# Optimization experiments

Measured on AMD Instinct MI355X. Metric: run time of the kernel, lower is better.

Reference implementation:

```python
import jax, jax.numpy as jnp
import numpy as np

EMB = 1024
NH = 16
DH = EMB // NH
SCALE = np.sqrt(EMB).astype(np.float32)  # module scales by sqrt(emb_dim), not sqrt(d_head)


def setup_inputs() -> dict:
    key = jax.random.key(0)
    ks = jax.random.split(key, 9)
    s = 1.0 / np.sqrt(EMB)
    return {
        "a": jax.random.normal(ks[0], (4, 2048, EMB), jnp.float32),
        "Wq": jax.random.normal(ks[1], (EMB, EMB), jnp.float32) * s,
        "bq": jnp.zeros((EMB,), jnp.float32),
        "Wk": jax.random.normal(ks[2], (EMB, EMB), jnp.float32) * s,
        "bk": jnp.zeros((EMB,), jnp.float32),
        "Wv": jax.random.normal(ks[3], (EMB, EMB), jnp.float32) * s,
        "bv": jnp.zeros((EMB,), jnp.float32),
        "Wo": jax.random.normal(ks[4], (EMB, EMB), jnp.float32) * s,
        "bo": jnp.zeros((EMB,), jnp.float32),
    }


def reference(a, Wq, bq, Wk, bk, Wv, bv, Wo, bo):
    N, S, _ = a.shape
    # Q/K/V projections (self-attention: b is None -> b = a)
    Q = (a @ Wq + bq).reshape(N, S, NH, DH).transpose(0, 2, 1, 3)  # [N,H,A,D]
    K = (a @ Wk + bk).reshape(N, S, NH, DH).transpose(0, 2, 1, 3)  # [N,H,B,D]
    V = (a @ Wv + bv).reshape(N, S, NH, DH).transpose(0, 2, 1, 3)  # [N,H,B,D]
    score = jnp.einsum('nhad,nhbd->nhab', Q, K) / SCALE
    score = jax.nn.softmax(score, axis=-1)
    out = jnp.einsum('nhab,nhbd->nhad', score, V)                  # [N,H,A,D]
    out = out.transpose(0, 2, 1, 3).reshape(N, S, EMB)
    return out @ Wo + bo
```

## Files before the change

kernel.cpp:

```cpp
#include <hip/hip_runtime.h>
#include <hip/hip_bf16.h>
#include <stdint.h>

typedef __attribute__((ext_vector_type(8))) short short8v;
typedef __attribute__((ext_vector_type(4))) float float4v;

#define GLDS16(gp, lp) __builtin_amdgcn_global_load_lds( \
    (const __attribute__((address_space(1))) void*)(gp),  \
    (__attribute__((address_space(3))) void*)(lp), 16, 0, 0)

#if __has_builtin(__builtin_amdgcn_exp2f)
#define EXP2(x) __builtin_amdgcn_exp2f(x)
#else
#define EXP2(x) exp2f(x)
#endif

#define LOG2E 1.4426950408889634f

__global__ __launch_bounds__(256) void cast_a_kernel(
    const float* __restrict__ src, __hip_bfloat16* __restrict__ dst, int n4) {
  int i = blockIdx.x * blockDim.x + threadIdx.x;
  if (i < n4) {
    float4 v = ((const float4*)src)[i];
    union { __hip_bfloat16 h[4]; ushort4 u; } p;
    p.h[0] = __float2bfloat16(v.x);
    p.h[1] = __float2bfloat16(v.y);
    p.h[2] = __float2bfloat16(v.z);
    p.h[3] = __float2bfloat16(v.w);
    ((ushort4*)dst)[i] = p.u;
  }
}

__global__ __launch_bounds__(256) void transpose_cast_kernel(
    const float* __restrict__ W, __hip_bfloat16* __restrict__ WT) {
  __shared__ float t[32][33];
  int tx = threadIdx.x & 31, ty = threadIdx.x >> 5;
  int r0 = blockIdx.y * 32, c0 = blockIdx.x * 32;
#pragma unroll
  for (int i = 0; i < 4; ++i) {
    int r = ty + i * 8;
    t[r][tx] = W[(size_t)(r0 + r) * 1024 + c0 + tx];
  }
  __syncthreads();
#pragma unroll
  for (int i = 0; i < 4; ++i) {
    int r = ty + i * 8;
    WT[(size_t)(c0 + r) * 1024 + r0 + tx] = __float2bfloat16(t[tx][r]);
  }
}

template <int MODE>
__global__ __launch_bounds__(256, 2) void gemm_kernel(
    const __hip_bfloat16* __restrict__ A, const __hip_bfloat16* __restrict__ BT,
    const float* __restrict__ bias, void* __restrict__ C, float scale) {
  __shared__ char lds[16384];
  const int tid = threadIdx.x;
  const int l = tid & 63, w = tid >> 6;
  const int g = l >> 4, cc = l & 15;
  const int m0 = blockIdx.x * 128, n0 = blockIdx.y * 128;
  const int wm = w >> 1, wn = w & 1;

  float4v acc[4][4];
#pragma unroll
  for (int m = 0; m < 4; ++m)
#pragma unroll
    for (int n = 0; n < 4; ++n) acc[m][n] = (float4v){0.f, 0.f, 0.f, 0.f};

  for (int kt = 0; kt < 32; ++kt) {
#pragma unroll
    for (int j = 0; j < 2; ++j) {
      int ci = (w * 2 + j) * 64 + l;
      int row = ci >> 2, ko = (ci & 3) * 16;
      GLDS16((const char*)A + (size_t)(m0 + row) * 2048 + kt * 64 + ko,
             lds + ci * 16);
      GLDS16((const char*)BT + (size_t)(n0 + row) * 2048 + kt * 64 + ko,
             lds + 8192 + ci * 16);
    }
    __syncthreads();
    short8v af[4], bf[4];
#pragma unroll
    for (int m = 0; m < 4; ++m)
      af[m] = *(const short8v*)(lds + ((wm * 64 + m * 16 + cc) * 32 + g * 8) * 2);
#pragma unroll
    for (int n = 0; n < 4; ++n)
      bf[n] = *(const short8v*)(lds + 8192 + ((wn * 64 + n * 16 + cc) * 32 + g * 8) * 2);
#pragma unroll
    for (int m = 0; m < 4; ++m)
#pragma unroll
      for (int n = 0; n < 4; ++n)
        acc[m][n] = __builtin_amdgcn_mfma_f32_16x16x32_bf16(af[m], bf[n], acc[m][n], 0, 0, 0);
    __syncthreads();
  }

  if (MODE == 0) {
    float* out = (float*)C;
#pragma unroll
    for (int m = 0; m < 4; ++m) {
      int row = m0 + wm * 64 + m * 16 + g * 4;
#pragma unroll
      for (int n = 0; n < 4; ++n) {
        int col = n0 + wn * 64 + n * 16 + cc;
        float b = bias[col];
#pragma unroll
        for (int r = 0; r < 4; ++r)
          out[(size_t)(row + r) * 1024 + col] = acc[m][n][r] + b;
      }
    }
  } else if (MODE == 1) {
    __hip_bfloat16* out = (__hip_bfloat16*)C;
#pragma unroll
    for (int m = 0; m < 4; ++m) {
#pragma unroll
      for (int n = 0; n < 4; ++n) {
        int col = n0 + wn * 64 + n * 16 + cc;
        float b = bias[col];
        int h = col >> 6, d = col & 63;
#pragma unroll
        for (int r = 0; r < 4; ++r) {
          int grow = m0 + wm * 64 + m * 16 + g * 4 + r;
          int nb = grow >> 11, s = grow & 2047;
          out[((size_t)(nb * 16 + h) * 2048 + s) * 64 + d] =
              __float2bfloat16((acc[m][n][r] + b) * scale);
        }
      }
    }
  } else {
    __hip_bfloat16* out = (__hip_bfloat16*)C;
#pragma unroll
    for (int m = 0; m < 4; ++m) {
#pragma unroll
      for (int n = 0; n < 4; ++n) {
        int col = n0 + wn * 64 + n * 16 + cc;
        int nb = col >> 11, key = col & 2047;
        int kp = (key & ~31) | ((key & 12) << 1) | (((key >> 4) & 1) << 2) | (key & 3);
#pragma unroll
        for (int r = 0; r < 4; ++r) {
          int row = m0 + wm * 64 + m * 16 + g * 4 + r;
          int h = row >> 6, d = row & 63;
          out[((size_t)((nb * 16 + h) * 64 + d)) * 2048 + kp] =
              __float2bfloat16(acc[m][n][r] + bias[row]);
        }
      }
    }
  }
}

__global__ __launch_bounds__(256, 4) void attn_kernel(
    const __hip_bfloat16* __restrict__ Q,
    const __hip_bfloat16* __restrict__ K,
    const __hip_bfloat16* __restrict__ VT,
    __hip_bfloat16* __restrict__ AO) {
  __shared__ char sK[2][8192];
  __shared__ char sV[2][8192];
  const int tid = threadIdx.x;
  const int l = tid & 63, w = tid >> 6;
  const int g = l >> 4, cc = l & 15;
  const int bid = blockIdx.x;
  const int nbid = (bid & 7) * 128 + (bid >> 3);
  const int bx = nbid & 15, nh = nbid >> 4;
  const int q0 = bx * 128 + w * 32;
  const char* Kb = (const char*)(K + (size_t)nh * 131072);
  const char* Vb = (const char*)(VT + (size_t)nh * 131072);
  const __hip_bfloat16* Qb = Q + (size_t)nh * 131072;

  short8v qf[2][2];
#pragma unroll
  for (int qg = 0; qg < 2; ++qg)
#pragma unroll
    for (int dh = 0; dh < 2; ++dh)
      qf[qg][dh] = *(const short8v*)(Qb + (size_t)(q0 + qg * 16 + cc) * 64 + dh * 32 + g * 8);

  int koff[4][2], voff[4][2];
#pragma unroll
  for (int kg = 0; kg < 4; ++kg)
#pragma unroll
    for (int dh = 0; dh < 2; ++dh) {
      int row = kg * 16 + cc;
      koff[kg][dh] = (row * 128 + dh * 64 + g * 16) ^ ((row & 7) << 4);
    }
#pragma unroll
  for (int f = 0; f < 4; ++f)
#pragma unroll
    for (int hh = 0; hh < 2; ++hh) {
      int d = f * 16 + cc;
      voff[f][hh] = (d * 128 + hh * 64 + g * 16) ^ ((d & 7) << 4);
    }
  int stK[2], stV[2], stD[2];
#pragma unroll
  for (int ii = 0; ii < 2; ++ii) {
    int i = w + ii * 4;
    int s = i * 1024 + l * 16;
    int r = s >> 7;
    int off = (s & 127) ^ ((r & 7) << 4);
    stK[ii] = r * 128 + off;
    stV[ii] = r * 4096 + off;
    stD[ii] = i * 1024;
  }

  const short8v fone = {16256, 16256, 16256, 16256, 16256, 16256, 16256, 16256};

  float mr[2] = {0.f, 0.f}, lr[2] = {0.f, 0.f};
  float4v oacc[2][4];
#pragma unroll
  for (int qg = 0; qg < 2; ++qg)
#pragma unroll
    for (int f = 0; f < 4; ++f) oacc[qg][f] = (float4v){0.f, 0.f, 0.f, 0.f};

#define STAGE(b, ktv)                                                         \
  {                                                                           \
    _Pragma("unroll")                                                         \
    for (int ii = 0; ii < 2; ++ii) {                                          \
      GLDS16(Kb + (size_t)(ktv) * 8192 + stK[ii], sK[b] + stD[ii]);           \
      GLDS16(Vb + (size_t)(ktv) * 128 + stV[ii], sV[b] + stD[ii]);            \
    }                                                                         \
  }

  STAGE(0, 0);
  asm volatile("s_waitcnt vmcnt(0)" ::: "memory");
  __builtin_amdgcn_s_barrier();

#pragma unroll 2
  for (int kt = 0; kt < 32; ++kt) {
    const int cur = kt & 1;
    if (kt < 31) STAGE(cur ^ 1, kt + 1);
    const char* sKc = sK[cur];
    const char* sVc = sV[cur];

    short8v kf[4][2];
#pragma unroll
    for (int kg = 0; kg < 4; ++kg)
#pragma unroll
      for (int dh = 0; dh < 2; ++dh)
        kf[kg][dh] = *(const short8v*)(sKc + koff[kg][dh]);

    float4v sv[2][4];
    __builtin_amdgcn_s_setprio(1);
#pragma unroll
    for (int qg = 0; qg < 2; ++qg) {
      float nm = -mr[qg];
#pragma unroll
      for (int kg = 0; kg < 4; ++kg) {
        float4v z = (float4v){nm, nm, nm, nm};
        z = __builtin_amdgcn_mfma_f32_16x16x32_bf16(kf[kg][0], qf[qg][0], z, 0, 0, 0);
        sv[qg][kg] = __builtin_amdgcn_mfma_f32_16x16x32_bf16(kf[kg][1], qf[qg][1], z, 0, 0, 0);
      }
    }
    __builtin_amdgcn_s_setprio(0);

    short8v pf[2][2];
#pragma unroll
    for (int qg = 0; qg < 2; ++qg) {
      float t0 = fmaxf(fmaxf(sv[qg][0][0], sv[qg][0][1]), sv[qg][0][2]);
      float t1 = fmaxf(fmaxf(sv[qg][0][3], sv[qg][1][0]), sv[qg][1][1]);
      float t2 = fmaxf(fmaxf(sv[qg][1][2], sv[qg][1][3]), sv[qg][2][0]);
      float t3 = fmaxf(fmaxf(sv[qg][2][1], sv[qg][2][2]), sv[qg][2][3]);
      float t4 = fmaxf(fmaxf(sv[qg][3][0], sv[qg][3][1]), sv[qg][3][2]);
      float t5 = fmaxf(sv[qg][3][3], fmaxf(t0, t1));
      float vm = fmaxf(fmaxf(t2, t3), fmaxf(t4, t5));
      vm = fmaxf(vm, __shfl_xor(vm, 16));
      vm = fmaxf(vm, __shfl_xor(vm, 32));
      if (__any(vm > 11.54f)) {
        float rsc = EXP2(-vm);
        mr[qg] += vm;
        lr[qg] *= rsc;
#pragma unroll
        for (int f = 0; f < 4; ++f)
#pragma unroll
          for (int r = 0; r < 4; ++r) oacc[qg][f][r] *= rsc;
#pragma unroll
        for (int kg = 0; kg < 4; ++kg)
#pragma unroll
          for (int r = 0; r < 4; ++r) sv[qg][kg][r] -= vm;
      }
#pragma unroll
      for (int kg = 0; kg < 4; ++kg)
#pragma unroll
        for (int r = 0; r < 4; ++r) sv[qg][kg][r] = EXP2(sv[qg][kg][r]);
#pragma unroll
      for (int hh = 0; hh < 2; ++hh) {
        union { __hip_bfloat16 h[8]; short8v v8; } pk;
#pragma unroll
        for (int j = 0; j < 4; ++j) {
          pk.h[j]     = __float2bfloat16(sv[qg][2 * hh][j]);
          pk.h[4 + j] = __float2bfloat16(sv[qg][2 * hh + 1][j]);
        }
        pf[qg][hh] = pk.v8;
      }
      float4v t = (float4v){0.f, 0.f, 0.f, 0.f};
      t = __builtin_amdgcn_mfma_f32_16x16x32_bf16(fone, pf[qg][0], t, 0, 0, 0);
      t = __builtin_amdgcn_mfma_f32_16x16x32_bf16(fone, pf[qg][1], t, 0, 0, 0);
      lr[qg] += t[0];
    }

    __builtin_amdgcn_s_setprio(1);
#pragma unroll
    for (int f = 0; f < 4; ++f)
#pragma unroll
      for (int hh = 0; hh < 2; ++hh) {
        short8v vk = *(const short8v*)(sVc + voff[f][hh]);
#pragma unroll
        for (int qg = 0; qg < 2; ++qg)
          oacc[qg][f] = __builtin_amdgcn_mfma_f32_16x16x32_bf16(vk, pf[qg][hh], oacc[qg][f], 0, 0, 0);
      }
    __builtin_amdgcn_s_setprio(0);

    asm volatile("s_waitcnt vmcnt(0)" ::: "memory");
    __builtin_amdgcn_s_barrier();
  }
#undef STAGE

  int nb = nh >> 4, h = nh & 15;
#pragma unroll
  for (int qg = 0; qg < 2; ++qg) {
    float inv = 1.f / lr[qg];
    int qrow = q0 + qg * 16 + cc;
#pragma unroll
    for (int f = 0; f < 4; ++f)
#pragma unroll
      for (int r = 0; r < 4; ++r) {
        int d = f * 16 + g * 4 + r;
        AO[(size_t)(nb * 2048 + qrow) * 1024 + h * 64 + d] =
            __float2bfloat16(oacc[qg][f][r] * inv);
      }
  }
}

extern "C" void kernel_launch(void* const* d_in, const int* in_sizes, int n_in,
                              void* d_out, int out_size, void* d_ws, size_t ws_size,
                              hipStream_t stream) {
  const float* a  = (const float*)d_in[0];
  const float* Wq = (const float*)d_in[1];
  const float* bq = (const float*)d_in[2];
  const float* Wk = (const float*)d_in[3];
  const float* bk = (const float*)d_in[4];
  const float* Wv = (const float*)d_in[5];
  const float* bv = (const float*)d_in[6];
  const float* Wo = (const float*)d_in[7];
  const float* bo = (const float*)d_in[8];

  char* ws = (char*)d_ws;
  __hip_bfloat16* aB  = (__hip_bfloat16*)(ws);
  __hip_bfloat16* WqT = (__hip_bfloat16*)(ws + (16ull << 20));
  __hip_bfloat16* WkT = (__hip_bfloat16*)(ws + (18ull << 20));
  __hip_bfloat16* WvT = (__hip_bfloat16*)(ws + (20ull << 20));
  __hip_bfloat16* WoT = (__hip_bfloat16*)(ws + (22ull << 20));
  __hip_bfloat16* Qh  = (__hip_bfloat16*)(ws + (24ull << 20));
  __hip_bfloat16* Kh  = (__hip_bfloat16*)(ws + (40ull << 20));
  __hip_bfloat16* Vt  = (__hip_bfloat16*)(ws + (56ull << 20));
  __hip_bfloat16* AOb = (__hip_bfloat16*)(ws + (72ull << 20));

  cast_a_kernel<<<8192, 256, 0, stream>>>(a, aB, 8192 * 1024 / 4);
  dim3 tg(32, 32);
  transpose_cast_kernel<<<tg, 256, 0, stream>>>(Wq, WqT);
  transpose_cast_kernel<<<tg, 256, 0, stream>>>(Wk, WkT);
  transpose_cast_kernel<<<tg, 256, 0, stream>>>(Wv, WvT);
  transpose_cast_kernel<<<tg, 256, 0, stream>>>(Wo, WoT);

  dim3 gg(64, 8);
  gemm_kernel<1><<<gg, 256, 0, stream>>>(aB, WqT, bq, (void*)Qh, LOG2E / 32.f);
  gemm_kernel<1><<<gg, 256, 0, stream>>>(aB, WkT, bk, (void*)Kh, 1.f);
  dim3 gv(8, 64);
  gemm_kernel<2><<<gv, 256, 0, stream>>>(WvT, aB, bv, (void*)Vt, 1.f);

  attn_kernel<<<1024, 256, 0, stream>>>(Qh, Kh, Vt, AOb);

  gemm_kernel<0><<<gg, 256, 0, stream>>>(AOb, WoT, bo, d_out, 1.f);
}
```

Before: 215.9 us.

## Fuse QKV projections into one GEMM, batch weight transposes, triple-buffer attention

The four weight transpose launches become one launch with a z dimension, and the three Q/K/V projection GEMMs become a single launch over a concatenated weight. The V output is now computed as aB·Wv with packed 4-element bf16 stores into the permuted transposed layout. Both GEMMs get a swizzled block order for better L2 locality. The attention kernel moves from double to triple buffering with a partial vmcnt wait and one barrier per iteration, at the cost of more LDS and occupancy lowered from 4 to 3 blocks.

```diff
diff --git a/kernel.cpp b/kernel.cpp
--- a/kernel.cpp
+++ b/kernel.cpp
@@ -31,9 +31,14 @@
   }
 }
 
-__global__ __launch_bounds__(256) void transpose_cast_kernel(
-    const float* __restrict__ W, __hip_bfloat16* __restrict__ WT) {
+__global__ __launch_bounds__(256) void transpose4_kernel(
+    const float* __restrict__ Wq, const float* __restrict__ Wk,
+    const float* __restrict__ Wv, const float* __restrict__ Wo,
+    __hip_bfloat16* __restrict__ Wcat, __hip_bfloat16* __restrict__ WoT) {
   __shared__ float t[32][33];
+  const int z = blockIdx.z;
+  const float* W = (z == 0) ? Wq : (z == 1) ? Wk : (z == 2) ? Wv : Wo;
+  __hip_bfloat16* dst = (z < 3) ? (Wcat + (size_t)z * 1048576) : WoT;
   int tx = threadIdx.x & 31, ty = threadIdx.x >> 5;
   int r0 = blockIdx.y * 32, c0 = blockIdx.x * 32;
 #pragma unroll
@@ -45,19 +50,22 @@
 #pragma unroll
   for (int i = 0; i < 4; ++i) {
     int r = ty + i * 8;
-    WT[(size_t)(c0 + r) * 1024 + r0 + tx] = __float2bfloat16(t[tx][r]);
-  }
-}
-
-template <int MODE>
-__global__ __launch_bounds__(256, 2) void gemm_kernel(
+    dst[(size_t)(c0 + r) * 1024 + r0 + tx] = __float2bfloat16(t[tx][r]);
+  }
+}
+
+__global__ __launch_bounds__(256, 2) void gemm_qkv_kernel(
     const __hip_bfloat16* __restrict__ A, const __hip_bfloat16* __restrict__ BT,
-    const float* __restrict__ bias, void* __restrict__ C, float scale) {
+    const float* __restrict__ bq, const float* __restrict__ bk,
+    const float* __restrict__ bv, __hip_bfloat16* __restrict__ Qh,
+    __hip_bfloat16* __restrict__ Kh, __hip_bfloat16* __restrict__ Vt) {
   __shared__ char lds[16384];
   const int tid = threadIdx.x;
   const int l = tid & 63, w = tid >> 6;
   const int g = l >> 4, cc = l & 15;
-  const int m0 = blockIdx.x * 128, n0 = blockIdx.y * 128;
+  const int bid = blockIdx.x;
+  const int nbid = (bid & 7) * 192 + (bid >> 3);
+  const int m0 = (nbid & 63) * 128, n0 = (nbid >> 6) * 128;
   const int wm = w >> 1, wn = w & 1;
 
   float4v acc[4][4];
@@ -92,29 +100,18 @@
     __syncthreads();
   }
 
-  if (MODE == 0) {
-    float* out = (float*)C;
+  const int sec = n0 >> 10;
+  if (sec < 2) {
+    __hip_bfloat16* out = sec == 0 ? Qh : Kh;
+    const float* bias = sec == 0 ? bq : bk;
+    const float scale = sec == 0 ? (LOG2E / 32.f) : 1.f;
 #pragma unroll
     for (int m = 0; m < 4; ++m) {
-      int row = m0 + wm * 64 + m * 16 + g * 4;
 #pragma unroll
       for (int n = 0; n < 4; ++n) {
-        int col = n0 + wn * 64 + n * 16 + cc;
-        float b = bias[col];
-#pragma unroll
-        for (int r = 0; r < 4; ++r)
-          out[(size_t)(row + r) * 1024 + col] = acc[m][n][r] + b;
-      }
-    }
-  } else if (MODE == 1) {
-    __hip_bfloat16* out = (__hip_bfloat16*)C;
-#pragma unroll
-    for (int m = 0; m < 4; ++m) {
-#pragma unroll
-      for (int n = 0; n < 4; ++n) {
-        int col = n0 + wn * 64 + n * 16 + cc;
-        float b = bias[col];
-        int h = col >> 6, d = col & 63;
+        int colc = (n0 + wn * 64 + n * 16 + cc) & 1023;
+        float b = bias[colc];
+        int h = colc >> 6, d = colc & 63;
 #pragma unroll
         for (int r = 0; r < 4; ++r) {
           int grow = m0 + wm * 64 + m * 16 + g * 4 + r;
@@ -125,33 +122,90 @@
       }
     }
   } else {
-    __hip_bfloat16* out = (__hip_bfloat16*)C;
 #pragma unroll
     for (int m = 0; m < 4; ++m) {
+      int grow0 = m0 + wm * 64 + m * 16 + g * 4;
+      int nb = grow0 >> 11, key0 = grow0 & 2047;
+      int kp0 = (key0 & ~31) | ((key0 & 12) << 1) | (((key0 >> 4) & 1) << 2);
 #pragma unroll
       for (int n = 0; n < 4; ++n) {
-        int col = n0 + wn * 64 + n * 16 + cc;
-        int nb = col >> 11, key = col & 2047;
-        int kp = (key & ~31) | ((key & 12) << 1) | (((key >> 4) & 1) << 2) | (key & 3);
-#pragma unroll
-        for (int r = 0; r < 4; ++r) {
-          int row = m0 + wm * 64 + m * 16 + g * 4 + r;
-          int h = row >> 6, d = row & 63;
-          out[((size_t)((nb * 16 + h) * 64 + d)) * 2048 + kp] =
-              __float2bfloat16(acc[m][n][r] + bias[row]);
-        }
-      }
-    }
-  }
-}
-
-__global__ __launch_bounds__(256, 4) void attn_kernel(
+        int colc = (n0 + wn * 64 + n * 16 + cc) & 1023;
+        float b = bv[colc];
+        int h = colc >> 6, d = colc & 63;
+        union { __hip_bfloat16 h4[4]; uint2 u; } pk;
+#pragma unroll
+        for (int r = 0; r < 4; ++r) pk.h4[r] = __float2bfloat16(acc[m][n][r] + b);
+        *(uint2*)&Vt[((size_t)((nb * 16 + h) * 64 + d)) * 2048 + kp0] = pk.u;
+      }
+    }
+  }
+}
+
+__global__ __launch_bounds__(256, 2) void gemm_o_kernel(
+    const __hip_bfloat16* __restrict__ A, const __hip_bfloat16* __restrict__ BT,
+    const float* __restrict__ bias, float* __restrict__ C) {
+  __shared__ char lds[16384];
+  const int tid = threadIdx.x;
+  const int l = tid & 63, w = tid >> 6;
+  const int g = l >> 4, cc = l & 15;
+  const int bid = blockIdx.x;
+  const int nbid = (bid & 7) * 64 + (bid >> 3);
+  const int m0 = (nbid & 63) * 128, n0 = (nbid >> 6) * 128;
+  const int wm = w >> 1, wn = w & 1;
+
+  float4v acc[4][4];
+#pragma unroll
+  for (int m = 0; m < 4; ++m)
+#pragma unroll
+    for (int n = 0; n < 4; ++n) acc[m][n] = (float4v){0.f, 0.f, 0.f, 0.f};
+
+  for (int kt = 0; kt < 32; ++kt) {
+#pragma unroll
+    for (int j = 0; j < 2; ++j) {
+      int ci = (w * 2 + j) * 64 + l;
+      int row = ci >> 2, ko = (ci & 3) * 16;
+      GLDS16((const char*)A + (size_t)(m0 + row) * 2048 + kt * 64 + ko,
+             lds + ci * 16);
+      GLDS16((const char*)BT + (size_t)(n0 + row) * 2048 + kt * 64 + ko,
+             lds + 8192 + ci * 16);
+    }
+    __syncthreads();
+    short8v af[4], bf[4];
+#pragma unroll
+    for (int m = 0; m < 4; ++m)
+      af[m] = *(const short8v*)(lds + ((wm * 64 + m * 16 + cc) * 32 + g * 8) * 2);
+#pragma unroll
+    for (int n = 0; n < 4; ++n)
+      bf[n] = *(const short8v*)(lds + 8192 + ((wn * 64 + n * 16 + cc) * 32 + g * 8) * 2);
+#pragma unroll
+    for (int m = 0; m < 4; ++m)
+#pragma unroll
+      for (int n = 0; n < 4; ++n)
+        acc[m][n] = __builtin_amdgcn_mfma_f32_16x16x32_bf16(af[m], bf[n], acc[m][n], 0, 0, 0);
+    __syncthreads();
+  }
+
+#pragma unroll
+  for (int m = 0; m < 4; ++m) {
+    int row = m0 + wm * 64 + m * 16 + g * 4;
+#pragma unroll
+    for (int n = 0; n < 4; ++n) {
+      int col = n0 + wn * 64 + n * 16 + cc;
+      float b = bias[col];
+#pragma unroll
+      for (int r = 0; r < 4; ++r)
+        C[(size_t)(row + r) * 1024 + col] = acc[m][n][r] + b;
+    }
+  }
+}
+
+__global__ __launch_bounds__(256, 3) void attn_kernel(
     const __hip_bfloat16* __restrict__ Q,
     const __hip_bfloat16* __restrict__ K,
     const __hip_bfloat16* __restrict__ VT,
     __hip_bfloat16* __restrict__ AO) {
-  __shared__ char sK[2][8192];
-  __shared__ char sV[2][8192];
+  __shared__ char sK[3][8192];
+  __shared__ char sV[3][8192];
   const int tid = threadIdx.x;
   const int l = tid & 63, w = tid >> 6;
   const int g = l >> 4, cc = l & 15;
@@ -206,25 +260,30 @@
 #pragma unroll
     for (int f = 0; f < 4; ++f) oacc[qg][f] = (float4v){0.f, 0.f, 0.f, 0.f};
 
-#define STAGE(b, ktv)                                                         \
+#define STAGE(kb, vb, ktv)                                                    \
   {                                                                           \
     _Pragma("unroll")                                                         \
     for (int ii = 0; ii < 2; ++ii) {                                          \
-      GLDS16(Kb + (size_t)(ktv) * 8192 + stK[ii], sK[b] + stD[ii]);           \
-      GLDS16(Vb + (size_t)(ktv) * 128 + stV[ii], sV[b] + stD[ii]);            \
+      GLDS16(Kb + (size_t)(ktv) * 8192 + stK[ii], (kb) + stD[ii]);            \
+      GLDS16(Vb + (size_t)(ktv) * 128 + stV[ii], (vb) + stD[ii]);             \
     }                                                                         \
   }
 
-  STAGE(0, 0);
-  asm volatile("s_waitcnt vmcnt(0)" ::: "memory");
-  __builtin_amdgcn_s_barrier();
-
-#pragma unroll 2
+  char *k0 = sK[0], *k1 = sK[1], *k2 = sK[2];
+  char *v0 = sV[0], *v1 = sV[1], *v2 = sV[2];
+  STAGE(k0, v0, 0);
+  STAGE(k1, v1, 1);
+
   for (int kt = 0; kt < 32; ++kt) {
-    const int cur = kt & 1;
-    if (kt < 31) STAGE(cur ^ 1, kt + 1);
-    const char* sKc = sK[cur];
-    const char* sVc = sV[cur];
+    if (kt < 31) {
+      asm volatile("s_waitcnt vmcnt(4)" ::: "memory");
+    } else {
+      asm volatile("s_waitcnt vmcnt(0)" ::: "memory");
+    }
+    __builtin_amdgcn_s_barrier();
+    if (kt < 30) STAGE(k2, v2, kt + 2);
+    const char* sKc = k0;
+    const char* sVc = v0;
 
     short8v kf[4][2];
 #pragma unroll
@@ -304,8 +363,9 @@
       }
     __builtin_amdgcn_s_setprio(0);
 
-    asm volatile("s_waitcnt vmcnt(0)" ::: "memory");
-    __builtin_amdgcn_s_barrier();
+    char* tt;
+    tt = k0; k0 = k1; k1 = k2; k2 = tt;
+    tt = v0; v0 = v1; v1 = v2; v2 = tt;
   }
 #undef STAGE
 
@@ -339,30 +399,21 @@
   const float* bo = (const float*)d_in[8];
 
   char* ws = (char*)d_ws;
-  __hip_bfloat16* aB  = (__hip_bfloat16*)(ws);
-  __hip_bfloat16* WqT = (__hip_bfloat16*)(ws + (16ull << 20));
-  __hip_bfloat16* WkT = (__hip_bfloat16*)(ws + (18ull << 20));
-  __hip_bfloat16* WvT = (__hip_bfloat16*)(ws + (20ull << 20));
-  __hip_bfloat16* WoT = (__hip_bfloat16*)(ws + (22ull << 20));
-  __hip_bfloat16* Qh  = (__hip_bfloat16*)(ws + (24ull << 20));
-  __hip_bfloat16* Kh  = (__hip_bfloat16*)(ws + (40ull << 20));
-  __hip_bfloat16* Vt  = (__hip_bfloat16*)(ws + (56ull << 20));
-  __hip_bfloat16* AOb = (__hip_bfloat16*)(ws + (72ull << 20));
+  __hip_bfloat16* aB   = (__hip_bfloat16*)(ws);
+  __hip_bfloat16* Wcat = (__hip_bfloat16*)(ws + (16ull << 20));
+  __hip_bfloat16* WoT  = (__hip_bfloat16*)(ws + (22ull << 20));
+  __hip_bfloat16* Qh   = (__hip_bfloat16*)(ws + (24ull << 20));
+  __hip_bfloat16* Kh   = (__hip_bfloat16*)(ws + (40ull << 20));
+  __hip_bfloat16* Vt   = (__hip_bfloat16*)(ws + (56ull << 20));
+  __hip_bfloat16* AOb  = (__hip_bfloat16*)(ws + (72ull << 20));
 
   cast_a_kernel<<<8192, 256, 0, stream>>>(a, aB, 8192 * 1024 / 4);
-  dim3 tg(32, 32);
-  transpose_cast_kernel<<<tg, 256, 0, stream>>>(Wq, WqT);
-  transpose_cast_kernel<<<tg, 256, 0, stream>>>(Wk, WkT);
-  transpose_cast_kernel<<<tg, 256, 0, stream>>>(Wv, WvT);
-  transpose_cast_kernel<<<tg, 256, 0, stream>>>(Wo, WoT);
-
-  dim3 gg(64, 8);
-  gemm_kernel<1><<<gg, 256, 0, stream>>>(aB, WqT, bq, (void*)Qh, LOG2E / 32.f);
-  gemm_kernel<1><<<gg, 256, 0, stream>>>(aB, WkT, bk, (void*)Kh, 1.f);
-  dim3 gv(8, 64);
-  gemm_kernel<2><<<gv, 256, 0, stream>>>(WvT, aB, bv, (void*)Vt, 1.f);
+  dim3 tg(32, 32, 4);
+  transpose4_kernel<<<tg, 256, 0, stream>>>(Wq, Wk, Wv, Wo, Wcat, WoT);
+
+  gemm_qkv_kernel<<<1536, 256, 0, stream>>>(aB, Wcat, bq, bk, bv, Qh, Kh, Vt);
 
   attn_kernel<<<1024, 256, 0, stream>>>(Qh, Kh, Vt, AOb);
 
-  gemm_kernel<0><<<gg, 256, 0, stream>>>(AOb, WoT, bo, d_out, 1.f);
-}
+  gemm_o_kernel<<<512, 256, 0, stream>>>(AOb, WoT, bo, (float*)d_out);
+}
```

Result: faster. 207.8 us (-3.8%).
